# Optimization experiments

Hardware: AMD Instinct MI355X
Metric: run time of the kernel (lower is better)

## Reference

```python
import jax, jax.numpy as jnp
import numpy as np

B, S, H, UNITS = 32, 2048, 1024, 1024

def setup_inputs() -> dict:
    key = jax.random.key(0)
    ks = jax.random.split(key, 8)
    sc_h = 1.0 / np.sqrt(H)
    sc_u = 1.0 / np.sqrt(UNITS)
    return {
        "query": jax.random.normal(ks[0], (B, H), jnp.float32),
        "values": jax.random.normal(ks[1], (B, S, H), jnp.float32),
        "W1": jax.random.normal(ks[2], (H, UNITS), jnp.float32) * sc_h,
        "b1": jnp.zeros((UNITS,), jnp.float32),
        "W2": jax.random.normal(ks[3], (H, UNITS), jnp.float32) * sc_h,
        "b2": jnp.zeros((UNITS,), jnp.float32),
        "V": jax.random.normal(ks[4], (UNITS, 1), jnp.float32) * sc_u,
        "bv": jnp.zeros((1,), jnp.float32),
    }

def reference(query, values, W1, b1, W2, b2, V, bv):
    # W1(values): [B,S,U]; W2(query)[:,None,:]: [B,1,U] broadcast-added
    proj = jnp.tanh(
        jnp.einsum("bsh,hu->bsu", values, W1) + b1
        + (query @ W2 + b2)[:, None, :]
    )
    score = proj @ V + bv                      # [B,S,1]
    attention_weights = jax.nn.softmax(score, axis=1)  # softmax over seq
    context_vector = jnp.sum(attention_weights * values, axis=1)  # [B,H]
    return context_vector, attention_weights
```

## Files before the change

kernel.cpp:

```cpp
#include <hip/hip_runtime.h>
#include <hip/hip_bf16.h>


#define B_ 32
#define S_ 2048
#define H_ 1024
#define U_ 1024
#define M_ (B_ * S_)
#define NT_ 32

typedef __bf16 bf16;
typedef __bf16 bf16x8 __attribute__((ext_vector_type(8)));
typedef float  f32x4  __attribute__((ext_vector_type(4)));

__device__ __forceinline__ void gl2lds16(const void* g, void* l) {
    __builtin_amdgcn_global_load_lds(
        (const __attribute__((address_space(1))) void*)g,
        (__attribute__((address_space(3))) void*)l, 16, 0, 0);
}

__device__ __forceinline__ bf16x8 cvt8(float4 a, float4 b) {
    bf16x8 o;
    o[0] = (bf16)a.x; o[1] = (bf16)a.y; o[2] = (bf16)a.z; o[3] = (bf16)a.w;
    o[4] = (bf16)b.x; o[5] = (bf16)b.y; o[6] = (bf16)b.z; o[7] = (bf16)b.w;
    return o;
}

__global__ void prep_kernel(const float* __restrict__ W1, bf16* __restrict__ W1T,
                            const float* __restrict__ query, const float* __restrict__ W2,
                            const float* __restrict__ b2, float* __restrict__ q2,
                            const float* __restrict__ values, bf16* __restrict__ vbf) {
    __shared__ __align__(16) char smem[64 * 65 * 2];
    int tid = threadIdx.x;
    if (blockIdx.x < 256) {
        bf16* t = (bf16*)smem;
        int h0 = (blockIdx.x >> 4) * 64, u0 = (blockIdx.x & 15) * 64;
        #pragma unroll
        for (int i = 0; i < 16; ++i) {
            int idx = i * 256 + tid;
            int r = idx >> 6, c = idx & 63;
            t[c * 65 + r] = (bf16)W1[(long)(h0 + r) * U_ + u0 + c];
        }
        __syncthreads();
        #pragma unroll
        for (int i = 0; i < 16; ++i) {
            int idx = i * 256 + tid;
            int r = idx >> 6, c = idx & 63;
            W1T[(long)(u0 + r) * H_ + h0 + c] = t[r * 65 + c];
        }
    } else if (blockIdx.x < 768) {
        float* qsh  = (float*)smem;
        float* part = (float*)(smem + 4096);
        int idx = blockIdx.x - 256;
        int b  = idx >> 4;
        int u0 = (idx & 15) * 64;
        int ul = tid & 63, kc = tid >> 6;
        for (int i = tid; i < H_; i += 256) qsh[i] = query[b * H_ + i];
        __syncthreads();
        float acc = 0.f;
        const float* wp = W2 + (long)(kc * 256) * U_ + u0 + ul;
        #pragma unroll 8
        for (int h = 0; h < 256; ++h) acc += qsh[kc * 256 + h] * wp[(long)h * U_];
        part[kc * 64 + ul] = acc;
        __syncthreads();
        if (tid < 64)
            q2[b * U_ + u0 + tid] = part[tid] + part[64 + tid] + part[128 + tid]
                                    + part[192 + tid] + b2[u0 + tid];
    } else {
        long cid = (long)(blockIdx.x - 768) * 256 + tid;
        const long stride = 4096L * 256;
        const long n8 = (long)M_ * H_ / 8;
        for (long c = cid; c < n8; c += stride) {
            const float4* s = reinterpret_cast<const float4*>(values + c * 8);
            float4 a = s[0], b = s[1];
            *reinterpret_cast<bf16x8*>(vbf + c * 8) = cvt8(a, b);
        }
    }
}

__global__ __launch_bounds__(512, 2) void score_gemm8(
    const bf16* __restrict__ A,
    const bf16* __restrict__ BT,
    const float* __restrict__ b1, const float* __restrict__ q2,
    const float* __restrict__ V, float* __restrict__ score )
{
    __shared__ __align__(16) bf16 lds[65536];
    const int tid  = threadIdx.x;
    const int lane = tid & 63;
    const int wave = tid >> 6;
    const int wm = wave >> 2, wn = wave & 3;
    const int lrow = lane & 15, quad = lane >> 4;

    const int xcd = blockIdx.x & 7;
    const int j   = blockIdx.x >> 3;
    const int mt  = xcd * 32 + (j >> 2);
    const int nt  = j & 3;
    const long m0 = (long)mt * 256;
    const int  n0 = nt * 256;

    const int rs = wave * 16 + (lane >> 2);
    const int sl = (lane & 3) ^ ((lane >> 3) & 3);
    const bf16* a0  = A  + (m0 + rs) * H_ + sl * 8;
    const bf16* a1  = a0 + 128 * H_;
    const bf16* bt0 = BT + (long)(n0 + rs) * H_ + sl * 8;
    const bf16* bt1 = bt0 + 128 * H_;

    const int kse  = (quad ^ ((lrow >> 1) & 3)) * 8;
    const int aoff = (wm * 128 + lrow) * 32 + kse;
    const int boff = 8192 + (wn * 64 + lrow) * 32 + kse;

    f32x4 acc[8][4];
    const f32x4 zero = {0.f, 0.f, 0.f, 0.f};
    #pragma unroll
    for (int mi = 0; mi < 8; ++mi)
        #pragma unroll
        for (int ni = 0; ni < 4; ++ni) acc[mi][ni] = zero;

    for (int tt = 0; tt < 3; ++tt) {
        bf16* d = lds + tt * 16384 + wave * 512;
        gl2lds16(a0  + tt * 32, d);
        gl2lds16(a1  + tt * 32, d + 4096);
        gl2lds16(bt0 + tt * 32, d + 8192);
        gl2lds16(bt1 + tt * 32, d + 8192 + 4096);
    }
    __builtin_amdgcn_sched_barrier(0);
    asm volatile("s_waitcnt vmcnt(8)" ::: "memory");
    __builtin_amdgcn_s_barrier();
    __builtin_amdgcn_sched_barrier(0);

    #pragma unroll 1
    for (int t = 0; t < NT_; ++t) {
        const bf16* buf = lds + (t & 3) * 16384;
        if (t + 3 < NT_) {
            bf16* d = lds + ((t + 3) & 3) * 16384 + wave * 512;
            gl2lds16(a0 + (t + 3) * 32, d);
            gl2lds16(a1 + (t + 3) * 32, d + 4096);
        }
        bf16x8 af[4], bg[4];
        #pragma unroll
        for (int ni = 0; ni < 4; ++ni)
            bg[ni] = *reinterpret_cast<const bf16x8*>(buf + boff + ni * 512);
        #pragma unroll
        for (int mi = 0; mi < 4; ++mi)
            af[mi] = *reinterpret_cast<const bf16x8*>(buf + aoff + mi * 512);
        __builtin_amdgcn_s_setprio(1);
        #pragma unroll
        for (int mi = 0; mi < 4; ++mi)
            #pragma unroll
            for (int ni = 0; ni < 4; ++ni)
                acc[mi][ni] = __builtin_amdgcn_mfma_f32_16x16x32_bf16(
                    af[mi], bg[ni], acc[mi][ni], 0, 0, 0);
        __builtin_amdgcn_s_setprio(0);
        __builtin_amdgcn_sched_barrier(0);
        __builtin_amdgcn_s_barrier();
        __builtin_amdgcn_sched_barrier(0);
        if (t + 3 < NT_) {
            bf16* d = lds + ((t + 3) & 3) * 16384 + 8192 + wave * 512;
            gl2lds16(bt0 + (t + 3) * 32, d);
            gl2lds16(bt1 + (t + 3) * 32, d + 4096);
        }
        #pragma unroll
        for (int mi = 0; mi < 4; ++mi)
            af[mi] = *reinterpret_cast<const bf16x8*>(buf + aoff + (4 + mi) * 512);
        __builtin_amdgcn_s_setprio(1);
        #pragma unroll
        for (int mi = 0; mi < 4; ++mi)
            #pragma unroll
            for (int ni = 0; ni < 4; ++ni)
                acc[4 + mi][ni] = __builtin_amdgcn_mfma_f32_16x16x32_bf16(
                    af[mi], bg[ni], acc[4 + mi][ni], 0, 0, 0);
        __builtin_amdgcn_s_setprio(0);
        __builtin_amdgcn_sched_barrier(0);
        if (t < NT_ - 3)       asm volatile("s_waitcnt vmcnt(8)" ::: "memory");
        else if (t == NT_ - 3) asm volatile("s_waitcnt vmcnt(4)" ::: "memory");
        else if (t == NT_ - 2) asm volatile("s_waitcnt vmcnt(0)" ::: "memory");
        __builtin_amdgcn_s_barrier();
        __builtin_amdgcn_sched_barrier(0);
    }

    const int bb = (int)(m0 / S_);
    float bq[4], vv[4];
    #pragma unroll
    for (int ni = 0; ni < 4; ++ni) {
        int u = n0 + wn * 64 + ni * 16 + lrow;
        bq[ni] = b1[u] + q2[bb * U_ + u];
        vv[ni] = V[u];
    }
    #pragma unroll
    for (int mi = 0; mi < 8; ++mi) {
        #pragma unroll
        for (int r = 0; r < 4; ++r) {
            float s = 0.f;
            #pragma unroll
            for (int ni = 0; ni < 4; ++ni) {
                float x = acc[mi][ni][r] + bq[ni];
                float th = 1.f - 2.f / (__expf(2.f * x) + 1.f);
                s += th * vv[ni];
            }
            s += __shfl_xor(s, 1); s += __shfl_xor(s, 2);
            s += __shfl_xor(s, 4); s += __shfl_xor(s, 8);
            if (lrow == 0)
                atomicAdd(score + m0 + wm * 128 + mi * 16 + quad * 4 + r, s);
        }
    }
}

#define ASTRIDE 40
__global__ __launch_bounds__(256, 3) void score_gemm(
    const float* __restrict__ A32,
    const bf16* __restrict__ BT,
    const float* __restrict__ b1, const float* __restrict__ q2,
    const float* __restrict__ V, float* __restrict__ score )
{
    __shared__ __align__(16) bf16 a_sh[2 * 128 * ASTRIDE];
    __shared__ __align__(16) bf16 b_sh[2 * 128 * 32];
    const int tid  = threadIdx.x;
    const int lane = tid & 63;
    const int wave = tid >> 6;
    const int wm = wave >> 1, wn = wave & 1;
    const int xcd = blockIdx.x & 7;
    const int i_  = blockIdx.x >> 3;
    const int nt  = i_ & 7;
    const int mt  = xcd * 64 + (i_ >> 3);
    const long m0 = (long)mt * 128;
    const int  n0 = nt * 128;
    const int lrow = lane & 15;
    const int quad = lane >> 4;
    const int arow = tid >> 1;
    const int aseg = tid & 1;

    f32x4 acc[4][4];
    const f32x4 zero = {0.f, 0.f, 0.f, 0.f};
    #pragma unroll
    for (int mi = 0; mi < 4; ++mi)
        #pragma unroll
        for (int ni = 0; ni < 4; ++ni) acc[mi][ni] = zero;

    const float* Abase = A32 + m0 * H_;
    const bf16*  Bbase = BT + (long)n0 * H_;

    for (int kt = 0; kt < H_; kt += 64) {
        #pragma unroll
        for (int i = 0; i < 4; ++i) {
            int g  = i * 4 + wave;
            int hs = g >> 3, q = g & 7;
            int row = q * 16 + (lane >> 2);
            int gc  = (lane & 3) ^ ((row >> 1) & 3);
            gl2lds16(Bbase + (long)row * H_ + kt + hs * 32 + gc * 8,
                     (void*)(b_sh + hs * 4096 + q * 512));
        }
        float4 av[2][4];
        #pragma unroll
        for (int hs = 0; hs < 2; ++hs) {
            const float4* src = reinterpret_cast<const float4*>(
                Abase + (long)arow * H_ + kt + hs * 32 + aseg * 16);
            av[hs][0] = src[0]; av[hs][1] = src[1];
            av[hs][2] = src[2]; av[hs][3] = src[3];
        }
        #pragma unroll
        for (int hs = 0; hs < 2; ++hs) {
            bf16* dst = a_sh + hs * (128 * ASTRIDE) + arow * ASTRIDE + aseg * 16;
            *reinterpret_cast<bf16x8*>(dst)     = cvt8(av[hs][0], av[hs][1]);
            *reinterpret_cast<bf16x8*>(dst + 8) = cvt8(av[hs][2], av[hs][3]);
        }
        __syncthreads();

        #pragma unroll
        for (int hs = 0; hs < 2; ++hs) {
            bf16x8 af[4], bg[4];
            #pragma unroll
            for (int mi = 0; mi < 4; ++mi) {
                int r = wm * 64 + mi * 16 + lrow;
                af[mi] = *reinterpret_cast<const bf16x8*>(
                    a_sh + hs * (128 * ASTRIDE) + r * ASTRIDE + quad * 8);
            }
            #pragma unroll
            for (int ni = 0; ni < 4; ++ni) {
                int r = wn * 64 + ni * 16 + lrow;
                int p = quad ^ ((r >> 1) & 3);
                bg[ni] = *reinterpret_cast<const bf16x8*>(
                    b_sh + hs * 4096 + r * 32 + p * 8);
            }
            #pragma unroll
            for (int mi = 0; mi < 4; ++mi)
                #pragma unroll
                for (int ni = 0; ni < 4; ++ni)
                    acc[mi][ni] = __builtin_amdgcn_mfma_f32_16x16x32_bf16(
                        af[mi], bg[ni], acc[mi][ni], 0, 0, 0);
        }
        __syncthreads();
    }

    const int bb = (int)(m0 / S_);
    float bq[4], vv[4];
    #pragma unroll
    for (int ni = 0; ni < 4; ++ni) {
        int u = n0 + wn * 64 + ni * 16 + lrow;
        bq[ni] = b1[u] + q2[bb * U_ + u];
        vv[ni] = V[u];
    }
    #pragma unroll
    for (int mi = 0; mi < 4; ++mi) {
        #pragma unroll
        for (int r = 0; r < 4; ++r) {
            float s = 0.f;
            #pragma unroll
            for (int ni = 0; ni < 4; ++ni) {
                float x = acc[mi][ni][r] + bq[ni];
                float t = 1.f - 2.f / (__expf(2.f * x) + 1.f);
                s += t * vv[ni];
            }
            s += __shfl_xor(s, 1); s += __shfl_xor(s, 2);
            s += __shfl_xor(s, 4); s += __shfl_xor(s, 8);
            if (lrow == 0)
                atomicAdd(score + m0 + wm * 64 + mi * 16 + quad * 4 + r, s);
        }
    }
}

__global__ void softmax_kernel(float* __restrict__ attn) {
    __shared__ float sh[S_];
    __shared__ float red[8];
    int b = blockIdx.x, tid = threadIdx.x;
    float* row = attn + (long)b * S_;
    float lmax = -1e30f;
    for (int i = tid; i < S_; i += 256) { float v = row[i]; sh[i] = v; lmax = fmaxf(lmax, v); }
    #pragma unroll
    for (int m = 32; m; m >>= 1) lmax = fmaxf(lmax, __shfl_xor(lmax, m));
    if ((tid & 63) == 0) red[tid >> 6] = lmax;
    __syncthreads();
    float gmax = fmaxf(fmaxf(red[0], red[1]), fmaxf(red[2], red[3]));
    float lsum = 0.f;
    for (int i = tid; i < S_; i += 256) { float e = __expf(sh[i] - gmax); sh[i] = e; lsum += e; }
    #pragma unroll
    for (int m = 32; m; m >>= 1) lsum += __shfl_xor(lsum, m);
    if ((tid & 63) == 0) red[4 + (tid >> 6)] = lsum;
    __syncthreads();
    float inv = 1.f / (red[4] + red[5] + red[6] + red[7]);
    for (int i = tid; i < S_; i += 256) row[i] = sh[i] * inv;
}

__global__ void context_kernel(const float* __restrict__ vals, const float* __restrict__ attn,
                               float* __restrict__ ctx ) {
    __shared__ float a_sh[128];
    int b = blockIdx.x >> 4;
    int sc = blockIdx.x & 15;
    int tid = threadIdx.x;
    if (tid < 128) a_sh[tid] = attn[(long)b * S_ + sc * 128 + tid];
    __syncthreads();
    const float* base = vals + ((long)b * S_ + sc * 128) * H_ + tid * 4;
    float ax = 0.f, ay = 0.f, az = 0.f, aw = 0.f;
    #pragma unroll 4
    for (int s = 0; s < 128; ++s) {
        float w = a_sh[s];
        float4 v = *reinterpret_cast<const float4*>(base + (long)s * H_);
        ax += w * v.x; ay += w * v.y; az += w * v.z; aw += w * v.w;
    }
    float* c = ctx + (long)b * H_ + tid * 4;
    atomicAdd(c + 0, ax); atomicAdd(c + 1, ay);
    atomicAdd(c + 2, az); atomicAdd(c + 3, aw);
}

extern "C" void kernel_launch(void* const* d_in, const int* in_sizes, int n_in,
                              void* d_out, int out_size, void* d_ws, size_t ws_size,
                              hipStream_t stream) {
    const float* query  = (const float*)d_in[0];
    const float* values = (const float*)d_in[1];
    const float* W1     = (const float*)d_in[2];
    const float* b1     = (const float*)d_in[3];
    const float* W2     = (const float*)d_in[4];
    const float* b2     = (const float*)d_in[5];
    const float* V      = (const float*)d_in[6];

    char* ws = (char*)d_ws;
    bf16*  w1t = (bf16*)ws;
    float* q2  = (float*)(ws + (size_t)U_ * H_ * 2);
    bf16*  vbf = (bf16*)(ws + (size_t)U_ * H_ * 2 + (size_t)B_ * U_ * 4);
    const size_t need = (size_t)U_ * H_ * 2 + (size_t)B_ * U_ * 4
                      + (size_t)M_ * H_ * 2;

    float* ctx  = (float*)d_out;
    float* attn = (float*)d_out + B_ * H_;

    hipMemsetAsync(d_out, 0, (size_t)(B_ * H_ + B_ * S_) * sizeof(float), stream);

    if (ws_size >= need) {
        prep_kernel <<<768 + 4096, 256, 0, stream>>>(W1, w1t, query, W2, b2, q2, values, vbf);
        score_gemm8 <<<1024,       512, 0, stream>>>(vbf, w1t, b1, q2, V, attn);
    } else {
        prep_kernel <<<768,        256, 0, stream>>>(W1, w1t, query, W2, b2, q2, values, vbf);
        score_gemm  <<<(M_ / 128) * 8, 256, 0, stream>>>(values, w1t, b1, q2, V, attn);
    }
    softmax_kernel<<<B_,      256, 0, stream>>>(attn);
    context_kernel<<<B_ * 16, 256, 0, stream>>>(values, attn, ctx);
}
```

Measured before the change: 609.7 us.

## Software-pipeline LDS fragment loads across K tiles with register double buffering

Restructures the GEMM main loop so the B fragments and first-half A fragments for the next K tile are read from LDS during the current tile's second MFMA phase. It uses ping-pong register sets via a macro unrolled by two. It also removes one barrier per tile and adjusts the vmcnt/lgkmcnt waits. The aim is to hide LDS read latency behind MFMA work and cut synchronisation. In exchange it raises register pressure and relies on hand-tuned waitcnt values, which could be wrong, especially since the barrier that protected the buffer being overwritten has been removed.

```diff
diff --git a/kernel.cpp b/kernel.cpp
--- a/kernel.cpp
+++ b/kernel.cpp
@@ -100,10 +100,10 @@
 
     const int rs = wave * 16 + (lane >> 2);
     const int sl = (lane & 3) ^ ((lane >> 3) & 3);
-    const bf16* a0  = A  + (m0 + rs) * H_ + sl * 8;
-    const bf16* a1  = a0 + 128 * H_;
-    const bf16* bt0 = BT + (long)(n0 + rs) * H_ + sl * 8;
-    const bf16* bt1 = bt0 + 128 * H_;
+    const bf16* ag0 = A  + (m0 + rs) * H_ + sl * 8;
+    const bf16* ag1 = ag0 + 128 * H_;
+    const bf16* bg0 = BT + (long)(n0 + rs) * H_ + sl * 8;
+    const bf16* bg1 = bg0 + 128 * H_;
 
     const int kse  = (quad ^ ((lrow >> 1) & 3)) * 8;
     const int aoff = (wm * 128 + lrow) * 32 + kse;
@@ -118,65 +118,90 @@
 
     for (int tt = 0; tt < 3; ++tt) {
         bf16* d = lds + tt * 16384 + wave * 512;
-        gl2lds16(a0  + tt * 32, d);
-        gl2lds16(a1  + tt * 32, d + 4096);
-        gl2lds16(bt0 + tt * 32, d + 8192);
-        gl2lds16(bt1 + tt * 32, d + 8192 + 4096);
+        gl2lds16(ag0 + tt * 32, d);
+        gl2lds16(ag1 + tt * 32, d + 4096);
+        gl2lds16(bg0 + tt * 32, d + 8192);
+        gl2lds16(bg1 + tt * 32, d + 8192 + 4096);
     }
     __builtin_amdgcn_sched_barrier(0);
     asm volatile("s_waitcnt vmcnt(8)" ::: "memory");
     __builtin_amdgcn_s_barrier();
     __builtin_amdgcn_sched_barrier(0);
 
+    bf16x8 bgA[4], a0A[4], bgB[4], a0B[4], af1[4];
+
+    #pragma unroll
+    for (int ni = 0; ni < 4; ++ni)
+        bgA[ni] = *reinterpret_cast<const bf16x8*>(lds + boff + ni * 512);
+    #pragma unroll
+    for (int mi = 0; mi < 4; ++mi)
+        a0A[mi] = *reinterpret_cast<const bf16x8*>(lds + aoff + mi * 512);
+
+#define TILE_BODY(T, bgC, a0C, bgN, a0N) do {                                   \
+    const int t_ = (T);                                                         \
+    const bf16* buf_ = lds + (t_ & 3) * 16384;                                  \
+     \
+    if (t_ + 3 < NT_) {                                                         \
+        bf16* d_ = lds + ((t_ + 3) & 3) * 16384 + wave * 512;                   \
+        gl2lds16(ag0 + (t_ + 3) * 32, d_);                                      \
+        gl2lds16(ag1 + (t_ + 3) * 32, d_ + 4096);                               \
+    }                                                                           \
+    _Pragma("unroll")                                                           \
+    for (int mi = 0; mi < 4; ++mi)                                              \
+        af1[mi] = *reinterpret_cast<const bf16x8*>(buf_ + aoff + (4+mi) * 512); \
+    asm volatile("s_waitcnt lgkmcnt(4)" ::: "memory");                          \
+    __builtin_amdgcn_sched_barrier(0);                                          \
+    __builtin_amdgcn_s_setprio(1);                                              \
+    _Pragma("unroll")                                                           \
+    for (int mi = 0; mi < 4; ++mi)                                              \
+        _Pragma("unroll")                                                       \
+        for (int ni = 0; ni < 4; ++ni)                                          \
+            acc[mi][ni] = __builtin_amdgcn_mfma_f32_16x16x32_bf16(              \
+                a0C[mi], bgC[ni], acc[mi][ni], 0, 0, 0);                        \
+    __builtin_amdgcn_s_setprio(0);                                              \
+    __builtin_amdgcn_sched_barrier(0);                                          \
+             \
+    if (t_ < NT_ - 3)       asm volatile("s_waitcnt vmcnt(6)" ::: "memory");    \
+    else if (t_ == NT_ - 3) asm volatile("s_waitcnt vmcnt(4)" ::: "memory");    \
+    else if (t_ == NT_ - 2) asm volatile("s_waitcnt vmcnt(0)" ::: "memory");    \
+    __builtin_amdgcn_s_barrier();                                               \
+    __builtin_amdgcn_sched_barrier(0);                                          \
+            \
+    if (t_ + 3 < NT_) {                                                         \
+        bf16* d_ = lds + ((t_ + 3) & 3) * 16384 + 8192 + wave * 512;            \
+        gl2lds16(bg0 + (t_ + 3) * 32, d_);                                      \
+        gl2lds16(bg1 + (t_ + 3) * 32, d_ + 4096);                               \
+    }                                                                           \
+    if (t_ + 1 < NT_) {                                                         \
+        const bf16* nb_ = lds + ((t_ + 1) & 3) * 16384;                         \
+        _Pragma("unroll")                                                       \
+        for (int ni = 0; ni < 4; ++ni)                                          \
+            bgN[ni] = *reinterpret_cast<const bf16x8*>(nb_ + boff + ni * 512);  \
+        _Pragma("unroll")                                                       \
+        for (int mi = 0; mi < 4; ++mi)                                          \
+            a0N[mi] = *reinterpret_cast<const bf16x8*>(nb_ + aoff + mi * 512);  \
+        asm volatile("s_waitcnt lgkmcnt(8)" ::: "memory");                      \
+    } else {                                                                    \
+        asm volatile("s_waitcnt lgkmcnt(0)" ::: "memory");                      \
+    }                                                                           \
+    __builtin_amdgcn_sched_barrier(0);                                          \
+    __builtin_amdgcn_s_setprio(1);                                              \
+    _Pragma("unroll")                                                           \
+    for (int mi = 0; mi < 4; ++mi)                                              \
+        _Pragma("unroll")                                                       \
+        for (int ni = 0; ni < 4; ++ni)                                          \
+            acc[4+mi][ni] = __builtin_amdgcn_mfma_f32_16x16x32_bf16(            \
+                af1[mi], bgC[ni], acc[4+mi][ni], 0, 0, 0);                      \
+    __builtin_amdgcn_s_setprio(0);                                              \
+    __builtin_amdgcn_sched_barrier(0);                                          \
+} while (0)
+
     #pragma unroll 1
-    for (int t = 0; t < NT_; ++t) {
-        const bf16* buf = lds + (t & 3) * 16384;
-        if (t + 3 < NT_) {
-            bf16* d = lds + ((t + 3) & 3) * 16384 + wave * 512;
-            gl2lds16(a0 + (t + 3) * 32, d);
-            gl2lds16(a1 + (t + 3) * 32, d + 4096);
-        }
-        bf16x8 af[4], bg[4];
-        #pragma unroll
-        for (int ni = 0; ni < 4; ++ni)
-            bg[ni] = *reinterpret_cast<const bf16x8*>(buf + boff + ni * 512);
-        #pragma unroll
-        for (int mi = 0; mi < 4; ++mi)
-            af[mi] = *reinterpret_cast<const bf16x8*>(buf + aoff + mi * 512);
-        __builtin_amdgcn_s_setprio(1);
-        #pragma unroll
-        for (int mi = 0; mi < 4; ++mi)
-            #pragma unroll
-            for (int ni = 0; ni < 4; ++ni)
-                acc[mi][ni] = __builtin_amdgcn_mfma_f32_16x16x32_bf16(
-                    af[mi], bg[ni], acc[mi][ni], 0, 0, 0);
-        __builtin_amdgcn_s_setprio(0);
-        __builtin_amdgcn_sched_barrier(0);
-        __builtin_amdgcn_s_barrier();
-        __builtin_amdgcn_sched_barrier(0);
-        if (t + 3 < NT_) {
-            bf16* d = lds + ((t + 3) & 3) * 16384 + 8192 + wave * 512;
-            gl2lds16(bt0 + (t + 3) * 32, d);
-            gl2lds16(bt1 + (t + 3) * 32, d + 4096);
-        }
-        #pragma unroll
-        for (int mi = 0; mi < 4; ++mi)
-            af[mi] = *reinterpret_cast<const bf16x8*>(buf + aoff + (4 + mi) * 512);
-        __builtin_amdgcn_s_setprio(1);
-        #pragma unroll
-        for (int mi = 0; mi < 4; ++mi)
-            #pragma unroll
-            for (int ni = 0; ni < 4; ++ni)
-                acc[4 + mi][ni] = __builtin_amdgcn_mfma_f32_16x16x32_bf16(
-                    af[mi], bg[ni], acc[4 + mi][ni], 0, 0, 0);
-        __builtin_amdgcn_s_setprio(0);
-        __builtin_amdgcn_sched_barrier(0);
-        if (t < NT_ - 3)       asm volatile("s_waitcnt vmcnt(8)" ::: "memory");
-        else if (t == NT_ - 3) asm volatile("s_waitcnt vmcnt(4)" ::: "memory");
-        else if (t == NT_ - 2) asm volatile("s_waitcnt vmcnt(0)" ::: "memory");
-        __builtin_amdgcn_s_barrier();
-        __builtin_amdgcn_sched_barrier(0);
-    }
+    for (int tp = 0; tp < NT_; tp += 2) {
+        TILE_BODY(tp,     bgA, a0A, bgB, a0B);
+        TILE_BODY(tp + 1, bgB, a0B, bgA, a0A);
+    }
+#undef TILE_BODY
 
     const int bb = (int)(m0 / S_);
     float bq[4], vv[4];
```

Result: faster. 592.1 us (-2.9%).
